# Kernel optimization log

Hardware: AMD Instinct MI355X
Metric: run time of the kernel (lower is better)

## Reference

```python
import jax, jax.numpy as jnp
import numpy as np

N = 65536      # number of nodes being updated
EMBED = 1024   # embed_size
G = 256        # g_size (per-head dim)
MLP = 256      # mlp_size
H = 4          # n_head


def setup_inputs() -> dict:
    key = jax.random.key(0)
    ks = jax.random.split(key, 8)
    s_in = 1.0 / np.sqrt(EMBED)
    s_g = 1.0 / np.sqrt(G)
    s_m = 1.0 / np.sqrt(MLP)
    s_hg = 1.0 / np.sqrt(H * G)
    return {
        "q": jax.random.normal(ks[0], (N, EMBED), jnp.float32),
        "rep": jax.random.normal(ks[1], (N, EMBED), jnp.float32),
        "Wq": jax.random.normal(ks[2], (EMBED, H * G), jnp.float32) * s_in,
        "Wk": jax.random.normal(ks[3], (EMBED, H * G), jnp.float32) * s_in,
        "Wv": jax.random.normal(ks[4], (EMBED, H * G), jnp.float32) * s_in,
        "W1": jax.random.normal(ks[5], (H, G, MLP), jnp.float32) * s_g,
        "b1": jnp.zeros((H, MLP), jnp.float32),
        "W2": jax.random.normal(ks[6], (H, MLP, G), jnp.float32) * s_m,
        "b2": jnp.zeros((H, G), jnp.float32),
        "Ws": jax.random.normal(ks[7], (H * G, EMBED), jnp.float32) * s_hg,
    }


def reference(q, rep, Wq, Wk, Wv, W1, b1, W2, b2, Ws):
    # Per-head Q/K/V projections: [N, E] -> [N, H, G]
    n = q.shape[0]
    Qh = (q @ Wq).reshape(n, H, G)
    Kh = (rep @ Wk).reshape(n, H, G)
    Vh = (rep @ Wv).reshape(n, H, G)
    # Elementwise scaled attention gate (Q, K are per-node vectors -> 2D attn)
    gate = jax.nn.sigmoid(Qh * Kh * (1.0 / np.sqrt(G)))
    z = gate * Vh  # [N, H, G]
    # Per-head MLP (num_mlp = 1 block): G -> MLP -> G with ReLU
    h1 = jax.nn.relu(jnp.einsum('nhg,hgm->nhm', z, W1) + b1)
    z2 = jnp.einsum('nhm,hmg->nhg', h1, W2) + b2
    update_gate = z2.reshape(n, H * G)
    # update_attn_scale (no bias) + fused residual: h = Q - K + proj(gate)
    h = q - rep + update_gate @ Ws
    return h
```

## Files before the change

### kernel.cpp

```cpp
#include <hip/hip_runtime.h>
#include <hip/hip_bf16.h>


typedef __attribute__((ext_vector_type(8))) short bf16x8;
typedef __attribute__((ext_vector_type(4))) float f32x4;
typedef __attribute__((ext_vector_type(4))) short short4v;

static __device__ __forceinline__ short f2b(float x) {
  __hip_bfloat16 h = __float2bfloat16(x);
  return __builtin_bit_cast(short, h);
}
static __device__ __forceinline__ float b2f(short s) {
  unsigned u = ((unsigned)(unsigned short)s) << 16;
  return __builtin_bit_cast(float, u);
}

static __device__ __forceinline__ void stage_half(
    const short* __restrict__ g, long ld, short* dst, int wave, int lane)
{
  const int rw = lane >> 2;
  const int gg = (lane & 3) ^ ((rw >> 1) & 3);
  const short* gl = g + (long)rw * ld + (gg << 3);
  #pragma unroll
  for (int j = 0; j < 2; ++j) {
    const int r0 = j * 128 + wave * 16;
    __builtin_amdgcn_global_load_lds(
        (const __attribute__((address_space(1))) void*)(gl + (long)r0 * ld),
        (__attribute__((address_space(3))) void*)(dst + r0 * 32),
        16, 0, 0);
  }
}

static __device__ __forceinline__ void stage_half128(
    const short* __restrict__ g, long ld, short* dst, int wave, int lane)
{
  const int rw = lane >> 2;
  const int gg = (lane & 3) ^ ((rw >> 1) & 3);
  const int r0 = wave * 16;
  __builtin_amdgcn_global_load_lds(
      (const __attribute__((address_space(1))) void*)(g + (long)(r0 + rw) * ld + (gg << 3)),
      (__attribute__((address_space(3))) void*)(dst + r0 * 32),
      16, 0, 0);
}

__global__ void cvt_bf16(const float* __restrict__ in, short* __restrict__ out, long n) {
  long i = ((long)blockIdx.x * blockDim.x + threadIdx.x) * 4;
  const long stride = (long)gridDim.x * blockDim.x * 4;
  for (; i < n; i += stride) {
    float4 v = *(const float4*)(in + i);
    short4v o = { f2b(v.x), f2b(v.y), f2b(v.z), f2b(v.w) };
    *(short4v*)(out + i) = o;
  }
}

__global__ void prep_weights(
    const float* __restrict__ Wq, const float* __restrict__ Wk, const float* __restrict__ Wv,
    const float* __restrict__ W1, const float* __restrict__ W2, const float* __restrict__ Ws,
    short* __restrict__ wqt, short* __restrict__ wkt, short* __restrict__ wvt,
    short* __restrict__ w1t, short* __restrict__ w2t, short* __restrict__ wst)
{
  const int job = blockIdx.z;
  const float* src; short* dst; int R, C;
  if (job < 3)       { src = (job==0)?Wq:((job==1)?Wk:Wv); dst = (job==0)?wqt:((job==1)?wkt:wvt); R = 1024; C = 1024; }
  else if (job == 3) { src = Ws; dst = wst; R = 1024; C = 1024; }
  else if (job < 8)  { int h = job-4; src = W1 + h*65536; dst = w1t + h*65536; R = 256; C = 256; }
  else               { int h = job-8; src = W2 + h*65536; dst = w2t + h*65536; R = 256; C = 256; }
  const int c0 = blockIdx.x * 32, r0 = blockIdx.y * 32;
  if (c0 >= C || r0 >= R) return;
  __shared__ float t[32][33];
  for (int i = threadIdx.y; i < 32; i += 8)
    t[i][threadIdx.x] = src[(long)(r0 + i) * C + c0 + threadIdx.x];
  __syncthreads();
  for (int i = threadIdx.y; i < 32; i += 8)
    dst[(long)(c0 + i) * R + r0 + threadIdx.x] = f2b(t[threadIdx.x][i]);
}

template <int KDIM, bool RELU, bool BIAS, bool RESID, bool SWZ>
__global__ __launch_bounds__(512, 2) void gemm_bf16(
    const short* __restrict__ A, long lda, long zsa,
    const short* __restrict__ Bt, long ldb, long zsb,
    void* __restrict__ outv, long ldc, long zsc,
    const float* __restrict__ bias, long zsbias,
    const short* __restrict__ qres, const short* __restrict__ rres)
{
  __shared__ __align__(16) short lA[2][2][8192];
  __shared__ __align__(16) short lB[2][2][8192];
  const int lane = threadIdx.x & 63, wave = threadIdx.x >> 6;
  const int wm = wave >> 2, wn = wave & 3;
  int bx = blockIdx.x, by = blockIdx.y;
  if (SWZ) {
    const int nbx = gridDim.x;
    const int flat = by * nbx + bx;
    const int chunk = (int)(gridDim.x * gridDim.y) >> 3;
    const int fid = (flat & 7) * chunk + (flat >> 3);
    bx = fid % nbx; by = fid / nbx;
  }
  const long bm = (long)by * 256;
  const int  bn = bx * 256;
  const int  zi = blockIdx.z;

  const short* Ab = A + (long)zi * zsa + bm * lda;
  const short* Bb = Bt + (long)zi * zsb + (long)bn * ldb;
  constexpr int NT = KDIM / 64;
  const int g0 = lane >> 4;
  const int arow = wm * 128 + (lane & 15);
  const int bcol = wn * 64 + (lane & 15);

  auto stA = [&](int buf, int ks, int t) {
    const int tc = t < NT ? t : NT - 1;
    stage_half(Ab + tc * 64 + ks * 32, lda, &lA[buf][ks][0], wave, lane);
  };
  auto stB = [&](int buf, int ks, int t) {
    const int tc = t < NT ? t : NT - 1;
    stage_half(Bb + tc * 64 + ks * 32, ldb, &lB[buf][ks][0], wave, lane);
  };

  stA(0, 0, 0); stB(0, 0, 0);
  stA(0, 1, 0); stB(0, 1, 0);
  asm volatile("s_waitcnt vmcnt(4)" ::: "memory");
  __builtin_amdgcn_s_barrier();

  f32x4 acc[8][4] = {};
  bf16x8 b[4];

#define PHASE(BUF, MH, KS, LOADB, STAGE_STMT, DOVM)                         \
  {                                                                         \
    const short* aS = &lA[BUF][KS][0];                                      \
    const short* bS = &lB[BUF][KS][0];                                      \
    if (LOADB) {                                                            \
      _Pragma("unroll")                                                     \
      for (int j = 0; j < 4; ++j) {                                         \
        const int c = bcol + j * 16;                                        \
        b[j] = *(const bf16x8*)(bS + c * 32 + (((g0 ^ (c >> 1)) & 3) << 3));\
      }                                                                     \
    }                                                                       \
    bf16x8 a[4];                                                            \
    _Pragma("unroll")                                                       \
    for (int i2 = 0; i2 < 4; ++i2) {                                        \
      const int r = arow + (MH) * 64 + i2 * 16;                             \
      a[i2] = *(const bf16x8*)(aS + r * 32 + (((g0 ^ (r >> 1)) & 3) << 3)); \
    }                                                                       \
    STAGE_STMT;                                                             \
    if (DOVM) asm volatile("s_waitcnt vmcnt(4)" ::: "memory");              \
    asm volatile("s_waitcnt lgkmcnt(0)" ::: "memory");                      \
    __builtin_amdgcn_s_barrier();                                           \
    __builtin_amdgcn_sched_barrier(0);                                      \
    __builtin_amdgcn_s_setprio(1);                                          \
    _Pragma("unroll")                                                       \
    for (int i2 = 0; i2 < 4; ++i2)                                          \
      _Pragma("unroll")                                                     \
      for (int j = 0; j < 4; ++j)                                           \
        acc[(MH) * 4 + i2][j] = __builtin_amdgcn_mfma_f32_16x16x32_bf16(    \
            a[i2], b[j], acc[(MH) * 4 + i2][j], 0, 0, 0);                   \
    __builtin_amdgcn_s_setprio(0);                                          \
    asm volatile("" ::: "memory");                                          \
  }

  for (int t = 0; t < NT; t += 2) {
    PHASE(0, 0, 0, true,  { stA(1, 0, t + 1); stB(1, 0, t + 1); }, false)
    PHASE(0, 1, 0, false, {}, true)
    PHASE(0, 0, 1, true,  { stA(1, 1, t + 1); stB(1, 1, t + 1); }, false)
    PHASE(0, 1, 1, false, {}, true)
    PHASE(1, 0, 0, true,  { stA(0, 0, t + 2); stB(0, 0, t + 2); }, false)
    PHASE(1, 1, 0, false, {}, true)
    PHASE(1, 0, 1, true,  { stA(0, 1, t + 2); stB(0, 1, t + 2); }, false)
    PHASE(1, 1, 1, false, {}, true)
  }
#undef PHASE

  #pragma unroll
  for (int i = 0; i < 8; ++i)
    #pragma unroll
    for (int j = 0; j < 4; ++j)
      #pragma unroll
      for (int r = 0; r < 4; ++r) {
        const int rl = wm * 128 + i * 16 + ((lane >> 4) << 2) + r;
        const int cl = wn * 64 + j * 16 + (lane & 15);
        float v = acc[i][j][r];
        if (BIAS) v += bias[(long)zi * zsbias + bn + cl];
        if (RELU) v = v > 0.0f ? v : 0.0f;
        const long row = bm + rl;
        const long gi = (long)zi * zsc + row * ldc + bn + cl;
        if (RESID) {
          ((float*)outv)[gi] = b2f(qres[gi]) - b2f(rres[gi]) + v;
        } else {
          ((short*)outv)[gi] = f2b(v);
        }
      }
}

__global__ __launch_bounds__(512, 2) void gemm_g23(
    const short* __restrict__ rb,
    const short* __restrict__ wkt,
    const short* __restrict__ wvt,
    const short* __restrict__ gh,
    short* __restrict__ zb)
{
  __shared__ __align__(16) short lA[2][2][8192];
  __shared__ __align__(16) short lK[2][2][4096];
  __shared__ __align__(16) short lV[2][2][4096];
  const int lane = threadIdx.x & 63, wave = threadIdx.x >> 6;
  const int wm = wave >> 2, wn = wave & 3;
  int bx = blockIdx.x, by = blockIdx.y;
  {
    const int flat = by * 8 + bx;
    const int chunk = (int)(gridDim.x * gridDim.y) >> 3;
    const int fid = (flat & 7) * chunk + (flat >> 3);
    bx = fid & 7; by = fid >> 3;
  }
  const long bm = (long)by * 256;
  const int  bn = bx * 128;

  const short* Ab = rb + bm * 1024;
  const short* Kb = wkt + (long)bn * 1024;
  const short* Vb = wvt + (long)bn * 1024;
  constexpr int NT = 16;
  const int g0 = lane >> 4;
  const int arow = wm * 128 + (lane & 15);
  const int bcol = wn * 32 + (lane & 15);

  auto stAll = [&](int buf, int ks, int t) {
    const int tc = t < NT ? t : NT - 1;
    stage_half(Ab + tc * 64 + ks * 32, 1024, &lA[buf][ks][0], wave, lane);
    stage_half128(Kb + tc * 64 + ks * 32, 1024, &lK[buf][ks][0], wave, lane);
    stage_half128(Vb + tc * 64 + ks * 32, 1024, &lV[buf][ks][0], wave, lane);
  };

  stAll(0, 0, 0);
  stAll(0, 1, 0);
  asm volatile("s_waitcnt vmcnt(4)" ::: "memory");
  __builtin_amdgcn_s_barrier();

  f32x4 ack[8][2] = {};
  f32x4 acv[8][2] = {};
  bf16x8 bk[2], bv[2];

#define PHASEG(BUF, MH, KS, LOADB, STAGE_STMT, DOVM)                        \
  {                                                                         \
    const short* aS = &lA[BUF][KS][0];                                      \
    if (LOADB) {                                                            \
      _Pragma("unroll")                                                     \
      for (int j = 0; j < 2; ++j) {                                         \
        const int c = bcol + j * 16;                                        \
        const int so = c * 32 + (((g0 ^ (c >> 1)) & 3) << 3);               \
        bk[j] = *(const bf16x8*)(&lK[BUF][KS][0] + so);                     \
        bv[j] = *(const bf16x8*)(&lV[BUF][KS][0] + so);                     \
      }                                                                     \
    }                                                                       \
    bf16x8 a[4];                                                            \
    _Pragma("unroll")                                                       \
    for (int i2 = 0; i2 < 4; ++i2) {                                        \
      const int r = arow + (MH) * 64 + i2 * 16;                             \
      a[i2] = *(const bf16x8*)(aS + r * 32 + (((g0 ^ (r >> 1)) & 3) << 3)); \
    }                                                                       \
    STAGE_STMT;                                                             \
    if (DOVM) asm volatile("s_waitcnt vmcnt(4)" ::: "memory");              \
    asm volatile("s_waitcnt lgkmcnt(0)" ::: "memory");                      \
    __builtin_amdgcn_s_barrier();                                           \
    __builtin_amdgcn_sched_barrier(0);                                      \
    __builtin_amdgcn_s_setprio(1);                                          \
    _Pragma("unroll")                                                       \
    for (int i2 = 0; i2 < 4; ++i2)                                          \
      _Pragma("unroll")                                                     \
      for (int j = 0; j < 2; ++j) {                                         \
        ack[(MH) * 4 + i2][j] = __builtin_amdgcn_mfma_f32_16x16x32_bf16(    \
            a[i2], bk[j], ack[(MH) * 4 + i2][j], 0, 0, 0);                  \
        acv[(MH) * 4 + i2][j] = __builtin_amdgcn_mfma_f32_16x16x32_bf16(    \
            a[i2], bv[j], acv[(MH) * 4 + i2][j], 0, 0, 0);                  \
      }                                                                     \
    __builtin_amdgcn_s_setprio(0);                                          \
    asm volatile("" ::: "memory");                                          \
  }

  for (int t = 0; t < NT; t += 2) {
    PHASEG(0, 0, 0, true,  stAll(1, 0, t + 1), false)
    PHASEG(0, 1, 0, false, {}, true)
    PHASEG(0, 0, 1, true,  stAll(1, 1, t + 1), false)
    PHASEG(0, 1, 1, false, {}, true)
    PHASEG(1, 0, 0, true,  stAll(0, 0, t + 2), false)
    PHASEG(1, 1, 0, false, {}, true)
    PHASEG(1, 0, 1, true,  stAll(0, 1, t + 2), false)
    PHASEG(1, 1, 1, false, {}, true)
  }
#undef PHASEG

  #pragma unroll
  for (int i = 0; i < 8; ++i)
    #pragma unroll
    for (int j = 0; j < 2; ++j)
      #pragma unroll
      for (int r = 0; r < 4; ++r) {
        const int rl = wm * 128 + i * 16 + ((lane >> 4) << 2) + r;
        const int cl = wn * 32 + j * 16 + (lane & 15);
        const long gi = (bm + rl) * 1024 + bn + cl;
        const float x = b2f(gh[gi]) * ack[i][j][r] * 0.0625f;
        const float gate = 1.0f / (1.0f + __expf(-x));
        zb[gi] = f2b(gate * acv[i][j][r]);
      }
}

extern "C" void kernel_launch(void* const* d_in, const int* in_sizes, int n_in,
                              void* d_out, int out_size, void* d_ws, size_t ws_size,
                              hipStream_t stream) {
  const float* q   = (const float*)d_in[0];
  const float* rep = (const float*)d_in[1];
  const float* Wq  = (const float*)d_in[2];
  const float* Wk  = (const float*)d_in[3];
  const float* Wv  = (const float*)d_in[4];
  const float* W1  = (const float*)d_in[5];
  const float* b1  = (const float*)d_in[6];
  const float* W2  = (const float*)d_in[7];
  const float* b2  = (const float*)d_in[8];
  const float* Ws  = (const float*)d_in[9];
  float* out = (float*)d_out;

  const long NE = 67108864L;
  char* ws = (char*)d_ws;
  short* qb  = (short*)(ws);
  short* rb  = (short*)(ws + NE * 2);
  short* gh  = (short*)(ws + NE * 4);
  short* zb  = (short*)(ws + NE * 6);
  short* h1b = gh;
  short* ugb = zb;
  char*  wp  = ws + NE * 8;
  short* wqt = (short*)(wp);
  short* wkt = (short*)(wp + 2097152);
  short* wvt = (short*)(wp + 4194304);
  short* wst = (short*)(wp + 6291456);
  short* w1t = (short*)(wp + 8388608);
  short* w2t = (short*)(wp + 8912896);

  cvt_bf16<<<4096, 256, 0, stream>>>(q,   qb, NE);
  cvt_bf16<<<4096, 256, 0, stream>>>(rep, rb, NE);
  prep_weights<<<dim3(32, 32, 12), dim3(32, 8), 0, stream>>>(
      Wq, Wk, Wv, W1, W2, Ws, wqt, wkt, wvt, w1t, w2t, wst);

  gemm_bf16<1024, false, false, false, true><<<dim3(4, 256), 512, 0, stream>>>(
      qb, 1024, 0, wqt, 1024, 0, gh, 1024, 0, nullptr, 0, nullptr, nullptr);
  gemm_g23<<<dim3(8, 256), 512, 0, stream>>>(rb, wkt, wvt, gh, zb);

  gemm_bf16<256, true, true, false, false><<<dim3(1, 256, 4), 512, 0, stream>>>(
      zb, 1024, 256, w1t, 256, 65536, h1b, 1024, 256, b1, 256, nullptr, nullptr);
  gemm_bf16<256, false, true, false, false><<<dim3(1, 256, 4), 512, 0, stream>>>(
      h1b, 1024, 256, w2t, 256, 65536, ugb, 1024, 256, b2, 256, nullptr, nullptr);
  gemm_bf16<1024, false, false, true, true><<<dim3(4, 256), 512, 0, stream>>>(
      ugb, 1024, 0, wst, 1024, 0, out, 1024, 0, nullptr, 0, qb, rb);
}
```

Measured before the change: 1.109 ms.

## Deepen GEMM LDS pipeline to four 32-wide K slots with three-ahead prefetch

Both GEMM kernels replace the double-buffered 64-wide K tiles (two halves each) with a ring of four 32-wide K slots, prefetching three slices ahead and spreading A and B/KV staging across the two M-half phases. Wait counts go from vmcnt(4) to vmcnt(8), and an extra barrier is added after each phase's MFMAs, with the first barrier moved before the lgkmcnt wait. The goal is to hide more global load latency behind MFMA work, at the cost of more barriers per K step and the same LDS footprint.

```diff
diff --git a/kernel.cpp b/kernel.cpp
--- a/kernel.cpp
+++ b/kernel.cpp
@@ -83,8 +83,8 @@
     const float* __restrict__ bias, long zsbias,
     const short* __restrict__ qres, const short* __restrict__ rres)
 {
-  __shared__ __align__(16) short lA[2][2][8192];
-  __shared__ __align__(16) short lB[2][2][8192];
+  __shared__ __align__(16) short lA[4][8192];
+  __shared__ __align__(16) short lB[4][8192];
   const int lane = threadIdx.x & 63, wave = threadIdx.x >> 6;
   const int wm = wave >> 2, wn = wave & 3;
   int bx = blockIdx.x, by = blockIdx.y;
@@ -101,32 +101,33 @@
 
   const short* Ab = A + (long)zi * zsa + bm * lda;
   const short* Bb = Bt + (long)zi * zsb + (long)bn * ldb;
-  constexpr int NT = KDIM / 64;
+  constexpr int NS = KDIM / 32;
   const int g0 = lane >> 4;
   const int arow = wm * 128 + (lane & 15);
   const int bcol = wn * 64 + (lane & 15);
 
-  auto stA = [&](int buf, int ks, int t) {
-    const int tc = t < NT ? t : NT - 1;
-    stage_half(Ab + tc * 64 + ks * 32, lda, &lA[buf][ks][0], wave, lane);
+  auto stA = [&](int slot, int s) {
+    const int sc = s < NS ? s : NS - 1;
+    stage_half(Ab + sc * 32, lda, &lA[slot][0], wave, lane);
   };
-  auto stB = [&](int buf, int ks, int t) {
-    const int tc = t < NT ? t : NT - 1;
-    stage_half(Bb + tc * 64 + ks * 32, ldb, &lB[buf][ks][0], wave, lane);
+  auto stB = [&](int slot, int s) {
+    const int sc = s < NS ? s : NS - 1;
+    stage_half(Bb + sc * 32, ldb, &lB[slot][0], wave, lane);
   };
 
-  stA(0, 0, 0); stB(0, 0, 0);
-  stA(0, 1, 0); stB(0, 1, 0);
-  asm volatile("s_waitcnt vmcnt(4)" ::: "memory");
+  stA(0, 0); stB(0, 0);
+  stA(1, 1); stB(1, 1);
+  stA(2, 2); stB(2, 2);
+  asm volatile("s_waitcnt vmcnt(8)" ::: "memory");
   __builtin_amdgcn_s_barrier();
 
   f32x4 acc[8][4] = {};
   bf16x8 b[4];
 
-#define PHASE(BUF, MH, KS, LOADB, STAGE_STMT, DOVM)                         \
+#define PHASE(SLOT, MH, LOADB, STAGE_STMT, DOVM)                            \
   {                                                                         \
-    const short* aS = &lA[BUF][KS][0];                                      \
-    const short* bS = &lB[BUF][KS][0];                                      \
+    const short* aS = &lA[SLOT][0];                                         \
+    const short* bS = &lB[SLOT][0];                                         \
     if (LOADB) {                                                            \
       _Pragma("unroll")                                                     \
       for (int j = 0; j < 4; ++j) {                                         \
@@ -141,9 +142,10 @@
       a[i2] = *(const bf16x8*)(aS + r * 32 + (((g0 ^ (r >> 1)) & 3) << 3)); \
     }                                                                       \
     STAGE_STMT;                                                             \
-    if (DOVM) asm volatile("s_waitcnt vmcnt(4)" ::: "memory");              \
+    if (DOVM) asm volatile("s_waitcnt vmcnt(8)" ::: "memory");              \
+    asm volatile("" ::: "memory");                                          \
+    __builtin_amdgcn_s_barrier();                                           \
     asm volatile("s_waitcnt lgkmcnt(0)" ::: "memory");                      \
-    __builtin_amdgcn_s_barrier();                                           \
     __builtin_amdgcn_sched_barrier(0);                                      \
     __builtin_amdgcn_s_setprio(1);                                          \
     _Pragma("unroll")                                                       \
@@ -154,17 +156,14 @@
             a[i2], b[j], acc[(MH) * 4 + i2][j], 0, 0, 0);                   \
     __builtin_amdgcn_s_setprio(0);                                          \
     asm volatile("" ::: "memory");                                          \
-  }
-
-  for (int t = 0; t < NT; t += 2) {
-    PHASE(0, 0, 0, true,  { stA(1, 0, t + 1); stB(1, 0, t + 1); }, false)
-    PHASE(0, 1, 0, false, {}, true)
-    PHASE(0, 0, 1, true,  { stA(1, 1, t + 1); stB(1, 1, t + 1); }, false)
-    PHASE(0, 1, 1, false, {}, true)
-    PHASE(1, 0, 0, true,  { stA(0, 0, t + 2); stB(0, 0, t + 2); }, false)
-    PHASE(1, 1, 0, false, {}, true)
-    PHASE(1, 0, 1, true,  { stA(0, 1, t + 2); stB(0, 1, t + 2); }, false)
-    PHASE(1, 1, 1, false, {}, true)
+    __builtin_amdgcn_s_barrier();                                           \
+  }
+
+  for (int s = 0; s < NS; s += 4) {
+    PHASE(0, 0, true,  stA(3, s + 3), false) PHASE(0, 1, false, stB(3, s + 3), true)
+    PHASE(1, 0, true,  stA(0, s + 4), false) PHASE(1, 1, false, stB(0, s + 4), true)
+    PHASE(2, 0, true,  stA(1, s + 5), false) PHASE(2, 1, false, stB(1, s + 5), true)
+    PHASE(3, 0, true,  stA(2, s + 6), false) PHASE(3, 1, false, stB(2, s + 6), true)
   }
 #undef PHASE
 
@@ -196,9 +195,9 @@
     const short* __restrict__ gh,
     short* __restrict__ zb)
 {
-  __shared__ __align__(16) short lA[2][2][8192];
-  __shared__ __align__(16) short lK[2][2][4096];
-  __shared__ __align__(16) short lV[2][2][4096];
+  __shared__ __align__(16) short lA[4][8192];
+  __shared__ __align__(16) short lK[4][4096];
+  __shared__ __align__(16) short lV[4][4096];
   const int lane = threadIdx.x & 63, wave = threadIdx.x >> 6;
   const int wm = wave >> 2, wn = wave & 3;
   int bx = blockIdx.x, by = blockIdx.y;
@@ -214,37 +213,41 @@
   const short* Ab = rb + bm * 1024;
   const short* Kb = wkt + (long)bn * 1024;
   const short* Vb = wvt + (long)bn * 1024;
-  constexpr int NT = 16;
+  constexpr int NS = 32;
   const int g0 = lane >> 4;
   const int arow = wm * 128 + (lane & 15);
   const int bcol = wn * 32 + (lane & 15);
 
-  auto stAll = [&](int buf, int ks, int t) {
-    const int tc = t < NT ? t : NT - 1;
-    stage_half(Ab + tc * 64 + ks * 32, 1024, &lA[buf][ks][0], wave, lane);
-    stage_half128(Kb + tc * 64 + ks * 32, 1024, &lK[buf][ks][0], wave, lane);
-    stage_half128(Vb + tc * 64 + ks * 32, 1024, &lV[buf][ks][0], wave, lane);
+  auto stA = [&](int slot, int s) {
+    const int sc = s < NS ? s : NS - 1;
+    stage_half(Ab + sc * 32, 1024, &lA[slot][0], wave, lane);
   };
-
-  stAll(0, 0, 0);
-  stAll(0, 1, 0);
-  asm volatile("s_waitcnt vmcnt(4)" ::: "memory");
+  auto stKV = [&](int slot, int s) {
+    const int sc = s < NS ? s : NS - 1;
+    stage_half128(Kb + sc * 32, 1024, &lK[slot][0], wave, lane);
+    stage_half128(Vb + sc * 32, 1024, &lV[slot][0], wave, lane);
+  };
+
+  stA(0, 0); stKV(0, 0);
+  stA(1, 1); stKV(1, 1);
+  stA(2, 2); stKV(2, 2);
+  asm volatile("s_waitcnt vmcnt(8)" ::: "memory");
   __builtin_amdgcn_s_barrier();
 
   f32x4 ack[8][2] = {};
   f32x4 acv[8][2] = {};
   bf16x8 bk[2], bv[2];
 
-#define PHASEG(BUF, MH, KS, LOADB, STAGE_STMT, DOVM)                        \
+#define PHASEG(SLOT, MH, LOADB, STAGE_STMT, DOVM)                           \
   {                                                                         \
-    const short* aS = &lA[BUF][KS][0];                                      \
+    const short* aS = &lA[SLOT][0];                                         \
     if (LOADB) {                                                            \
       _Pragma("unroll")                                                     \
       for (int j = 0; j < 2; ++j) {                                         \
         const int c = bcol + j * 16;                                        \
         const int so = c * 32 + (((g0 ^ (c >> 1)) & 3) << 3);               \
-        bk[j] = *(const bf16x8*)(&lK[BUF][KS][0] + so);                     \
-        bv[j] = *(const bf16x8*)(&lV[BUF][KS][0] + so);                     \
+        bk[j] = *(const bf16x8*)(&lK[SLOT][0] + so);                        \
+        bv[j] = *(const bf16x8*)(&lV[SLOT][0] + so);                        \
       }                                                                     \
     }                                                                       \
     bf16x8 a[4];                                                            \
@@ -254,9 +257,10 @@
       a[i2] = *(const bf16x8*)(aS + r * 32 + (((g0 ^ (r >> 1)) & 3) << 3)); \
     }                                                                       \
     STAGE_STMT;                                                             \
-    if (DOVM) asm volatile("s_waitcnt vmcnt(4)" ::: "memory");              \
+    if (DOVM) asm volatile("s_waitcnt vmcnt(8)" ::: "memory");              \
+    asm volatile("" ::: "memory");                                          \
+    __builtin_amdgcn_s_barrier();                                           \
     asm volatile("s_waitcnt lgkmcnt(0)" ::: "memory");                      \
-    __builtin_amdgcn_s_barrier();                                           \
     __builtin_amdgcn_sched_barrier(0);                                      \
     __builtin_amdgcn_s_setprio(1);                                          \
     _Pragma("unroll")                                                       \
@@ -270,17 +274,14 @@
       }                                                                     \
     __builtin_amdgcn_s_setprio(0);                                          \
     asm volatile("" ::: "memory");                                          \
-  }
-
-  for (int t = 0; t < NT; t += 2) {
-    PHASEG(0, 0, 0, true,  stAll(1, 0, t + 1), false)
-    PHASEG(0, 1, 0, false, {}, true)
-    PHASEG(0, 0, 1, true,  stAll(1, 1, t + 1), false)
-    PHASEG(0, 1, 1, false, {}, true)
-    PHASEG(1, 0, 0, true,  stAll(0, 0, t + 2), false)
-    PHASEG(1, 1, 0, false, {}, true)
-    PHASEG(1, 0, 1, true,  stAll(0, 1, t + 2), false)
-    PHASEG(1, 1, 1, false, {}, true)
+    __builtin_amdgcn_s_barrier();                                           \
+  }
+
+  for (int s = 0; s < NS; s += 4) {
+    PHASEG(0, 0, true,  stA(3, s + 3), false) PHASEG(0, 1, false, stKV(3, s + 3), true)
+    PHASEG(1, 0, true,  stA(0, s + 4), false) PHASEG(1, 1, false, stKV(0, s + 4), true)
+    PHASEG(2, 0, true,  stA(1, s + 5), false) PHASEG(2, 1, false, stKV(1, s + 5), true)
+    PHASEG(3, 0, true,  stA(2, s + 6), false) PHASEG(3, 1, false, stKV(2, s + 6), true)
   }
 #undef PHASEG
 
```

Measured after the change: 1.045 ms. 5.8% less time.
